# Optimization experiments

Measured on AMD Instinct MI355X. Metric: run time of the kernel, lower is better.

The kernel has to match this reference:

```python
import jax, jax.numpy as jnp
import numpy as np

LN_EPS = 1e-5


def setup_inputs() -> dict:
    key = jax.random.key(0)
    ks = jax.random.split(key, 8)
    N, H, E, D, B = 262144, 768, 768, 2048, 65536
    return {
        "u_t": jax.random.normal(ks[0], (B, E), dtype=jnp.float32),
        "s_i": jax.random.randint(ks[1], (B,), 0, N, dtype=jnp.int64),
        "speaker_embeddings": jax.random.normal(ks[2], (N, H), dtype=jnp.float32),
        "W1": jax.random.normal(ks[3], (D, H + E), dtype=jnp.float32) * 0.02,
        "b1": jax.random.normal(ks[4], (D,), dtype=jnp.float32) * 0.02,
        "W2": jax.random.normal(ks[5], (H, D), dtype=jnp.float32) * 0.02,
        "b2": jax.random.normal(ks[6], (H,), dtype=jnp.float32) * 0.02,
        "ln_gamma": jnp.ones((H,), dtype=jnp.float32),
        "ln_beta": jnp.zeros((H,), dtype=jnp.float32),
    }


def reference(u_t, s_i, speaker_embeddings, W1, b1, W2, b2, ln_gamma, ln_beta):
    # gather speaker vectors: [B, H]
    h_t = speaker_embeddings[s_i]
    # concat [u_t, h_t] along features: [B, E+H]
    x = jnp.concatenate([u_t, h_t], axis=-1)
    # Linear -> GELU (exact, torch default) -> (Dropout=identity in eval)
    h = jax.nn.gelu(jnp.einsum("bf,df->bd", x, W1) + b1, approximate=False)
    # Linear -> (Dropout=identity) : [B, H]
    y = jnp.einsum("bd,hd->bh", h, W2) + b2
    # LayerNorm over last dim
    mu = jnp.mean(y, axis=-1, keepdims=True)
    var = jnp.mean((y - mu) ** 2, axis=-1, keepdims=True)
    new_h_t = (y - mu) * jax.lax.rsqrt(var + LN_EPS) * ln_gamma + ln_beta
    # scatter-add back into the memory table (duplicates accumulate)
    updated = speaker_embeddings.at[s_i].add(new_h_t)
    return new_h_t, updated
```

## Files before the change

### kernel.cpp

```cpp
#include <hip/hip_runtime.h>
#include <hip/hip_bf16.h>

typedef unsigned short u16;
typedef unsigned int u32;
typedef short bf16x8 __attribute__((ext_vector_type(8)));
typedef float f32x4 __attribute__((ext_vector_type(4)));

__device__ __forceinline__ unsigned pk2(float lo, float hi) {
    unsigned a = (unsigned)__builtin_bit_cast(u16, __float2bfloat16(lo));
    unsigned b = (unsigned)__builtin_bit_cast(u16, __float2bfloat16(hi));
    return a | (b << 16);
}
__device__ __forceinline__ u16 f2bf(float v) {
    return __builtin_bit_cast(u16, __float2bfloat16(v));
}
__device__ __forceinline__ void gl_lds16(const u16* g, u16* l) {
    __builtin_amdgcn_global_load_lds(
        (const __attribute__((address_space(1))) u32*)g,
        (__attribute__((address_space(3))) u32*)l, 16, 0, 0);
}

__global__ void cvtbf(const float4* __restrict__ s, uint2* __restrict__ d, int n4) {
    int i = blockIdx.x * blockDim.x + threadIdx.x;
    int stride = gridDim.x * blockDim.x;
    for (; i < n4; i += stride) {
        float4 f = s[i];
        uint2 o;
        o.x = pk2(f.x, f.y);
        o.y = pk2(f.z, f.w);
        d[i] = o;
    }
}

__global__ __launch_bounds__(256) void xbuild(const float* __restrict__ u_t,
                                              const float* __restrict__ emb,
                                              const int* __restrict__ s_i,
                                              u16* __restrict__ xb) {
    const long u = (long)blockIdx.x * blockDim.x + threadIdx.x;
    const int row = (int)(u / 192);
    const int c8 = (int)(u % 192);
    const float* src = (c8 < 96) ? (u_t + (long)row * 768 + c8 * 8)
                                 : (emb + (long)s_i[row] * 768 + (c8 - 96) * 8);
    float4 f0 = ((const float4*)src)[0];
    float4 f1 = ((const float4*)src)[1];
    uint4 o;
    o.x = pk2(f0.x, f0.y);
    o.y = pk2(f0.z, f0.w);
    o.z = pk2(f1.x, f1.y);
    o.w = pk2(f1.z, f1.w);
    *(uint4*)(xb + u * 8) = o;
}

__global__ __launch_bounds__(256, 3) void gemm1_gelu(
    const u16* __restrict__ xb, const u16* __restrict__ w1b,
    const float* __restrict__ b1, u16* __restrict__ hbuf) {
    __shared__ __align__(16) u16 As[128 * 64];
    __shared__ __align__(16) u16 Bs[128 * 64];

    const int tid = threadIdx.x;
    const int lane = tid & 63;
    const int wv = tid >> 6;
    const int cpx = gridDim.x >> 3;
    const int tile = ((int)blockIdx.x & 7) * cpx + ((int)blockIdx.x >> 3);
    const int tm = tile >> 4;
    const int tn = tile & 15;
    const long rowBase = (long)tm * 128;
    const long colBase = (long)tn * 128;

    const u16* gA0 = xb + (rowBase + 8 * wv + (lane >> 3)) * 1536 + (lane & 7) * 8;
    const u16* gB0 = w1b + (colBase + 8 * wv + (lane >> 3)) * 1536 + (lane & 7) * 8;

    auto stage = [&](int kt) {
        const u16* ga = gA0 + kt * 64;
        const u16* gb = gB0 + kt * 64;
#pragma unroll
        for (int i = 0; i < 4; ++i) {
            gl_lds16(ga + (long)i * 32 * 1536, As + (32 * i + 8 * wv) * 64);
            gl_lds16(gb + (long)i * 32 * 1536, Bs + (32 * i + 8 * wv) * 64);
        }
    };

    const int wr = wv >> 1, wc = wv & 1;
    const u16* aBase = As + (wr * 64 + (lane & 15)) * 64 + (lane >> 4) * 8;
    const u16* bBase = Bs + (wc * 64 + (lane & 15)) * 64 + (lane >> 4) * 8;

    f32x4 acc[4][4];
    const f32x4 zero = {0.f, 0.f, 0.f, 0.f};
#pragma unroll
    for (int m = 0; m < 4; ++m)
#pragma unroll
        for (int n = 0; n < 4; ++n) acc[m][n] = zero;

    stage(0);
    for (int kt = 0; kt < 24; ++kt) {
        __syncthreads();
#pragma unroll
        for (int kk = 0; kk < 2; ++kk) {
            bf16x8 a[4], b[4];
#pragma unroll
            for (int m = 0; m < 4; ++m) a[m] = *(const bf16x8*)(aBase + m * 16 * 64 + kk * 32);
#pragma unroll
            for (int n = 0; n < 4; ++n) b[n] = *(const bf16x8*)(bBase + n * 16 * 64 + kk * 32);
#pragma unroll
            for (int m = 0; m < 4; ++m)
#pragma unroll
                for (int n = 0; n < 4; ++n)
                    acc[m][n] = __builtin_amdgcn_mfma_f32_16x16x32_bf16(a[m], b[n], acc[m][n], 0, 0, 0);
        }
        if (kt + 1 < 24) {
            __syncthreads();
            stage(kt + 1);
        }
    }

    const float* b1p = b1 + colBase;
#pragma unroll
    for (int n = 0; n < 4; ++n) {
        int gcl = wc * 64 + n * 16 + (lane & 15);
        float bias = b1p[gcl];
        long gc = colBase + gcl;
#pragma unroll
        for (int m = 0; m < 4; ++m) {
            long gr = rowBase + wr * 64 + m * 16 + ((lane >> 4) << 2);
            u16* dst = hbuf + gr * 2048 + gc;
#pragma unroll
            for (int j = 0; j < 4; ++j) {
                float v = acc[m][n][j] + bias;
                v = 0.5f * v * (1.0f + erff(v * 0.70710678118f));
                dst[(long)j * 2048] = f2bf(v);
            }
        }
    }
}

__global__ __launch_bounds__(256, 3) void gemm2_bias(
    const u16* __restrict__ hbuf, const u16* __restrict__ w2b,
    const float* __restrict__ b2, float* __restrict__ yout) {
    __shared__ __align__(16) u16 As[128 * 64];
    __shared__ __align__(16) u16 Bs[128 * 64];

    const int tid = threadIdx.x;
    const int lane = tid & 63;
    const int wv = tid >> 6;
    const int cpx = gridDim.x >> 3;
    const int tile = ((int)blockIdx.x & 7) * cpx + ((int)blockIdx.x >> 3);
    const int tm = tile / 6;
    const int tn = tile % 6;
    const long rowBase = (long)tm * 128;
    const long colBase = (long)tn * 128;

    const u16* gA0 = hbuf + (rowBase + 8 * wv + (lane >> 3)) * 2048 + (lane & 7) * 8;
    const u16* gB0 = w2b + (colBase + 8 * wv + (lane >> 3)) * 2048 + (lane & 7) * 8;

    auto stage = [&](int kt) {
        const u16* ga = gA0 + kt * 64;
        const u16* gb = gB0 + kt * 64;
#pragma unroll
        for (int i = 0; i < 4; ++i) {
            gl_lds16(ga + (long)i * 32 * 2048, As + (32 * i + 8 * wv) * 64);
            gl_lds16(gb + (long)i * 32 * 2048, Bs + (32 * i + 8 * wv) * 64);
        }
    };

    const int wr = wv >> 1, wc = wv & 1;
    const u16* aBase = As + (wr * 64 + (lane & 15)) * 64 + (lane >> 4) * 8;
    const u16* bBase = Bs + (wc * 64 + (lane & 15)) * 64 + (lane >> 4) * 8;

    f32x4 acc[4][4];
    const f32x4 zero = {0.f, 0.f, 0.f, 0.f};
#pragma unroll
    for (int m = 0; m < 4; ++m)
#pragma unroll
        for (int n = 0; n < 4; ++n) acc[m][n] = zero;

    stage(0);
    for (int kt = 0; kt < 32; ++kt) {
        __syncthreads();
#pragma unroll
        for (int kk = 0; kk < 2; ++kk) {
            bf16x8 a[4], b[4];
#pragma unroll
            for (int m = 0; m < 4; ++m) a[m] = *(const bf16x8*)(aBase + m * 16 * 64 + kk * 32);
#pragma unroll
            for (int n = 0; n < 4; ++n) b[n] = *(const bf16x8*)(bBase + n * 16 * 64 + kk * 32);
#pragma unroll
            for (int m = 0; m < 4; ++m)
#pragma unroll
                for (int n = 0; n < 4; ++n)
                    acc[m][n] = __builtin_amdgcn_mfma_f32_16x16x32_bf16(a[m], b[n], acc[m][n], 0, 0, 0);
        }
        if (kt + 1 < 32) {
            __syncthreads();
            stage(kt + 1);
        }
    }

    const float* b2p = b2 + colBase;
#pragma unroll
    for (int n = 0; n < 4; ++n) {
        int gcl = wc * 64 + n * 16 + (lane & 15);
        float bias = b2p[gcl];
        long gc = colBase + gcl;
#pragma unroll
        for (int m = 0; m < 4; ++m) {
            long gr = rowBase + wr * 64 + m * 16 + ((lane >> 4) << 2);
            float* dst = yout + gr * 768 + gc;
#pragma unroll
            for (int j = 0; j < 4; ++j) dst[(long)j * 768] = acc[m][n][j] + bias;
        }
    }
}

__global__ __launch_bounds__(256) void ln_scatter(float* __restrict__ y,
                                                  const float* __restrict__ gamma,
                                                  const float* __restrict__ beta,
                                                  const int* __restrict__ s_i,
                                                  float* __restrict__ upd) {
    const int lane = threadIdx.x & 63;
    const long row = (long)blockIdx.x * 4 + (threadIdx.x >> 6);
    const long base = row * 768;
    float v[12];
#pragma unroll
    for (int i = 0; i < 12; ++i) v[i] = y[base + i * 64 + lane];
    float s = 0.f, q = 0.f;
#pragma unroll
    for (int i = 0; i < 12; ++i) { s += v[i]; q += v[i] * v[i]; }
#pragma unroll
    for (int off = 32; off > 0; off >>= 1) {
        s += __shfl_xor(s, off, 64);
        q += __shfl_xor(q, off, 64);
    }
    const float mu = s * (1.f / 768.f);
    const float var = q * (1.f / 768.f) - mu * mu;
    const float inv = rsqrtf(var + 1e-5f);
    const long si = s_i[row];
#pragma unroll
    for (int i = 0; i < 12; ++i) {
        int c = i * 64 + lane;
        float r = (v[i] - mu) * inv * gamma[c] + beta[c];
        y[base + c] = r;
        atomicAdd(&upd[si * 768 + c], r);
    }
}

__global__ void copy4(const float4* __restrict__ s, float4* __restrict__ d, long n) {
    long i = (long)blockIdx.x * blockDim.x + threadIdx.x;
    long stride = (long)gridDim.x * blockDim.x;
    for (; i < n; i += stride) d[i] = s[i];
}

extern "C" void kernel_launch(void* const* d_in, const int* in_sizes, int n_in,
                              void* d_out, int out_size, void* d_ws, size_t ws_size,
                              hipStream_t stream) {
    const float* u_t = (const float*)d_in[0];
    const int* s_i = (const int*)d_in[1];
    const float* emb = (const float*)d_in[2];
    const float* W1 = (const float*)d_in[3];
    const float* b1 = (const float*)d_in[4];
    const float* W2 = (const float*)d_in[5];
    const float* b2 = (const float*)d_in[6];
    const float* gamma = (const float*)d_in[7];
    const float* beta = (const float*)d_in[8];

    float* out = (float*)d_out;
    float* newh = out;
    float* upd = out + 50331648L;

    u16* base = (u16*)upd;
    u16* hbuf = base;
    u16* xb = base + 134217728L;
    u16* w1b = base + 234881024L;
    u16* w2b = base + 238026752L;

    cvtbf<<<1024, 256, 0, stream>>>((const float4*)W1, (uint2*)w1b, 786432);
    cvtbf<<<1024, 256, 0, stream>>>((const float4*)W2, (uint2*)w2b, 393216);
    xbuild<<<49152, 256, 0, stream>>>(u_t, emb, s_i, xb);
    gemm1_gelu<<<8192, 256, 0, stream>>>(xb, w1b, b1, hbuf);
    gemm2_bias<<<3072, 256, 0, stream>>>(hbuf, w2b, b2, newh);
    copy4<<<2048, 256, 0, stream>>>((const float4*)emb, (float4*)upd, 50331648L);
    ln_scatter<<<16384, 256, 0, stream>>>(newh, gamma, beta, s_i, upd);
}
```

Baseline: 1.544 ms.

## Replace both GEMMs with 256x256-tile, 8-wave, double-buffered swizzled-LDS kernel

Both bf16 GEMMs move from 128x128 tiles with 4 waves to a templated 256x256-tile kernel with 8 waves, 128 KB of double-buffered LDS and XOR-swizzled layouts. The main loop is split into four sub-phases that interleave global-to-LDS prefetch of the next K tile with MFMA work, using explicit vmcnt/lgkmcnt waits, raw barriers and s_setprio. The aim is higher arithmetic intensity per LDS byte, fewer bank conflicts, and load latency hidden behind compute. In exchange the kernel uses many more registers and much more LDS, lowering occupancy, and relies on hand-tuned wait counts that could be fragile.

```diff
diff --git a/kernel.cpp b/kernel.cpp
--- a/kernel.cpp
+++ b/kernel.cpp
@@ -5,6 +5,11 @@
 typedef unsigned int u32;
 typedef short bf16x8 __attribute__((ext_vector_type(8)));
 typedef float f32x4 __attribute__((ext_vector_type(4)));
+
+#define BAR() asm volatile("s_barrier" ::: "memory")
+#define WAITV4() asm volatile("s_waitcnt vmcnt(4)" ::: "memory")
+#define WAITV0() asm volatile("s_waitcnt vmcnt(0)" ::: "memory")
+#define WAITL() asm volatile("s_waitcnt lgkmcnt(0)" ::: "memory")
 
 __device__ __forceinline__ unsigned pk2(float lo, float hi) {
     unsigned a = (unsigned)__builtin_bit_cast(u16, __float2bfloat16(lo));
@@ -51,162 +56,161 @@
     *(uint4*)(xb + u * 8) = o;
 }
 
-__global__ __launch_bounds__(256, 3) void gemm1_gelu(
-    const u16* __restrict__ xb, const u16* __restrict__ w1b,
-    const float* __restrict__ b1, u16* __restrict__ hbuf) {
-    __shared__ __align__(16) u16 As[128 * 64];
-    __shared__ __align__(16) u16 Bs[128 * 64];
+template <int LDK, int NT, int TN, int EPI>
+__global__ __launch_bounds__(512, 2) void gemm256(
+    const u16* __restrict__ Ag, const u16* __restrict__ Bg,
+    const float* __restrict__ bias, u16* __restrict__ outb,
+    float* __restrict__ outf) {
+    __shared__ __align__(16) u16 lds[65536];
 
     const int tid = threadIdx.x;
     const int lane = tid & 63;
     const int wv = tid >> 6;
-    const int cpx = gridDim.x >> 3;
+    const int wm = wv >> 2;
+    const int wn = wv & 3;
+
+    const int cpx = (int)gridDim.x >> 3;
     const int tile = ((int)blockIdx.x & 7) * cpx + ((int)blockIdx.x >> 3);
-    const int tm = tile >> 4;
-    const int tn = tile & 15;
-    const long rowBase = (long)tm * 128;
-    const long colBase = (long)tn * 128;
-
-    const u16* gA0 = xb + (rowBase + 8 * wv + (lane >> 3)) * 1536 + (lane & 7) * 8;
-    const u16* gB0 = w1b + (colBase + 8 * wv + (lane >> 3)) * 1536 + (lane & 7) * 8;
-
-    auto stage = [&](int kt) {
-        const u16* ga = gA0 + kt * 64;
-        const u16* gb = gB0 + kt * 64;
-#pragma unroll
-        for (int i = 0; i < 4; ++i) {
-            gl_lds16(ga + (long)i * 32 * 1536, As + (32 * i + 8 * wv) * 64);
-            gl_lds16(gb + (long)i * 32 * 1536, Bs + (32 * i + 8 * wv) * 64);
-        }
+    const int tm = tile / TN, tn = tile % TN;
+    const long rowBase = (long)tm * 256;
+    const long colBase = (long)tn * 256;
+
+    const int srow = tid >> 2;
+    const int gch = (tid & 3) ^ ((tid >> 3) & 3);
+    const u16* pA = Ag + (rowBase + srow) * (long)LDK + gch * 8;
+    const u16* pB = Bg + (colBase + srow) * (long)LDK + gch * 8;
+    const int dstBase = wv * 512;
+
+    auto stageA = [&](int kt, int ks, int b) {
+        const u16* s = pA + kt * 64 + ks * 32;
+        u16* d = lds + b * 32768 + ks * 8192 + dstBase;
+        gl_lds16(s, d);
+        gl_lds16(s + (long)128 * LDK, d + 4096);
     };
-
-    const int wr = wv >> 1, wc = wv & 1;
-    const u16* aBase = As + (wr * 64 + (lane & 15)) * 64 + (lane >> 4) * 8;
-    const u16* bBase = Bs + (wc * 64 + (lane & 15)) * 64 + (lane >> 4) * 8;
-
-    f32x4 acc[4][4];
+    auto stageB = [&](int kt, int ks, int b) {
+        const u16* s = pB + kt * 64 + ks * 32;
+        u16* d = lds + b * 32768 + 16384 + ks * 8192 + dstBase;
+        gl_lds16(s, d);
+        gl_lds16(s + (long)128 * LDK, d + 4096);
+    };
+
+    const int l15 = lane & 15, lc = lane >> 4;
+    int offA[8], offB[4];
+#pragma unroll
+    for (int i = 0; i < 8; ++i) {
+        int r = wm * 128 + i * 16 + l15;
+        offA[i] = r * 32 + ((lc ^ ((r >> 1) & 3)) << 3);
+    }
+#pragma unroll
+    for (int n = 0; n < 4; ++n) {
+        int r = wn * 64 + n * 16 + l15;
+        offB[n] = r * 32 + ((lc ^ ((r >> 1) & 3)) << 3);
+    }
+
+    f32x4 acc[8][4];
     const f32x4 zero = {0.f, 0.f, 0.f, 0.f};
 #pragma unroll
-    for (int m = 0; m < 4; ++m)
+    for (int m = 0; m < 8; ++m)
 #pragma unroll
         for (int n = 0; n < 4; ++n) acc[m][n] = zero;
 
-    stage(0);
-    for (int kt = 0; kt < 24; ++kt) {
-        __syncthreads();
-#pragma unroll
-        for (int kk = 0; kk < 2; ++kk) {
-            bf16x8 a[4], b[4];
-#pragma unroll
-            for (int m = 0; m < 4; ++m) a[m] = *(const bf16x8*)(aBase + m * 16 * 64 + kk * 32);
-#pragma unroll
-            for (int n = 0; n < 4; ++n) b[n] = *(const bf16x8*)(bBase + n * 16 * 64 + kk * 32);
-#pragma unroll
-            for (int m = 0; m < 4; ++m)
-#pragma unroll
-                for (int n = 0; n < 4; ++n)
-                    acc[m][n] = __builtin_amdgcn_mfma_f32_16x16x32_bf16(a[m], b[n], acc[m][n], 0, 0, 0);
-        }
-        if (kt + 1 < 24) {
-            __syncthreads();
-            stage(kt + 1);
-        }
-    }
-
-    const float* b1p = b1 + colBase;
+    stageA(0, 0, 0);
+    stageB(0, 0, 0);
+    stageA(0, 1, 0);
+    stageB(0, 1, 0);
+    WAITV4();
+    BAR();
+
+    bf16x8 bA[4], bB[4];
+    for (int kt = 0; kt < NT; ++kt) {
+        const int b = kt & 1;
+        const u16* rA0 = lds + b * 32768;
+        const u16* rB0 = rA0 + 16384;
+        const u16* rA1 = rA0 + 8192;
+        const u16* rB1 = rB0 + 8192;
+        const bool pf = (kt + 1 < NT);
+
+#pragma unroll
+        for (int n = 0; n < 4; ++n) bB[n] = *(const bf16x8*)(rB0 + offB[n]);
+#pragma unroll
+        for (int m = 0; m < 4; ++m) bA[m] = *(const bf16x8*)(rA0 + offA[m]);
+        if (pf) stageA(kt + 1, 0, b ^ 1);
+        BAR();
+        WAITL();
+        __builtin_amdgcn_s_setprio(1);
+#pragma unroll
+        for (int m = 0; m < 4; ++m)
+#pragma unroll
+            for (int n = 0; n < 4; ++n)
+                acc[m][n] = __builtin_amdgcn_mfma_f32_16x16x32_bf16(bA[m], bB[n], acc[m][n], 0, 0, 0);
+        __builtin_amdgcn_s_setprio(0);
+        BAR();
+
+#pragma unroll
+        for (int m = 0; m < 4; ++m) bA[m] = *(const bf16x8*)(rA0 + offA[4 + m]);
+        if (pf) stageB(kt + 1, 0, b ^ 1);
+        BAR();
+        WAITL();
+        __builtin_amdgcn_s_setprio(1);
+#pragma unroll
+        for (int m = 0; m < 4; ++m)
+#pragma unroll
+            for (int n = 0; n < 4; ++n)
+                acc[4 + m][n] = __builtin_amdgcn_mfma_f32_16x16x32_bf16(bA[m], bB[n], acc[4 + m][n], 0, 0, 0);
+        __builtin_amdgcn_s_setprio(0);
+        if (pf) { WAITV4(); } else { WAITV0(); }
+        BAR();
+
+#pragma unroll
+        for (int n = 0; n < 4; ++n) bB[n] = *(const bf16x8*)(rB1 + offB[n]);
+#pragma unroll
+        for (int m = 0; m < 4; ++m) bA[m] = *(const bf16x8*)(rA1 + offA[m]);
+        if (pf) stageA(kt + 1, 1, b ^ 1);
+        BAR();
+        WAITL();
+        __builtin_amdgcn_s_setprio(1);
+#pragma unroll
+        for (int m = 0; m < 4; ++m)
+#pragma unroll
+            for (int n = 0; n < 4; ++n)
+                acc[m][n] = __builtin_amdgcn_mfma_f32_16x16x32_bf16(bA[m], bB[n], acc[m][n], 0, 0, 0);
+        __builtin_amdgcn_s_setprio(0);
+        BAR();
+
+#pragma unroll
+        for (int m = 0; m < 4; ++m) bA[m] = *(const bf16x8*)(rA1 + offA[4 + m]);
+        if (pf) stageB(kt + 1, 1, b ^ 1);
+        BAR();
+        WAITL();
+        __builtin_amdgcn_s_setprio(1);
+#pragma unroll
+        for (int m = 0; m < 4; ++m)
+#pragma unroll
+            for (int n = 0; n < 4; ++n)
+                acc[4 + m][n] = __builtin_amdgcn_mfma_f32_16x16x32_bf16(bA[m], bB[n], acc[4 + m][n], 0, 0, 0);
+        __builtin_amdgcn_s_setprio(0);
+        if (pf) { WAITV4(); } else { WAITV0(); }
+        BAR();
+    }
+
+    const int N = TN * 256;
 #pragma unroll
     for (int n = 0; n < 4; ++n) {
-        int gcl = wc * 64 + n * 16 + (lane & 15);
-        float bias = b1p[gcl];
-        long gc = colBase + gcl;
-#pragma unroll
-        for (int m = 0; m < 4; ++m) {
-            long gr = rowBase + wr * 64 + m * 16 + ((lane >> 4) << 2);
-            u16* dst = hbuf + gr * 2048 + gc;
+        long gc = colBase + wn * 64 + n * 16 + l15;
+        float bv = bias[gc];
+#pragma unroll
+        for (int i = 0; i < 8; ++i) {
+            long gr = rowBase + wm * 128 + i * 16 + (lc << 2);
 #pragma unroll
             for (int j = 0; j < 4; ++j) {
-                float v = acc[m][n][j] + bias;
-                v = 0.5f * v * (1.0f + erff(v * 0.70710678118f));
-                dst[(long)j * 2048] = f2bf(v);
+                float v = acc[i][n][j] + bv;
+                if constexpr (EPI == 0) {
+                    v = 0.5f * v * (1.0f + erff(v * 0.70710678118f));
+                    outb[(gr + j) * N + gc] = f2bf(v);
+                } else {
+                    outf[(gr + j) * N + gc] = v;
+                }
             }
-        }
-    }
-}
-
-__global__ __launch_bounds__(256, 3) void gemm2_bias(
-    const u16* __restrict__ hbuf, const u16* __restrict__ w2b,
-    const float* __restrict__ b2, float* __restrict__ yout) {
-    __shared__ __align__(16) u16 As[128 * 64];
-    __shared__ __align__(16) u16 Bs[128 * 64];
-
-    const int tid = threadIdx.x;
-    const int lane = tid & 63;
-    const int wv = tid >> 6;
-    const int cpx = gridDim.x >> 3;
-    const int tile = ((int)blockIdx.x & 7) * cpx + ((int)blockIdx.x >> 3);
-    const int tm = tile / 6;
-    const int tn = tile % 6;
-    const long rowBase = (long)tm * 128;
-    const long colBase = (long)tn * 128;
-
-    const u16* gA0 = hbuf + (rowBase + 8 * wv + (lane >> 3)) * 2048 + (lane & 7) * 8;
-    const u16* gB0 = w2b + (colBase + 8 * wv + (lane >> 3)) * 2048 + (lane & 7) * 8;
-
-    auto stage = [&](int kt) {
-        const u16* ga = gA0 + kt * 64;
-        const u16* gb = gB0 + kt * 64;
-#pragma unroll
-        for (int i = 0; i < 4; ++i) {
-            gl_lds16(ga + (long)i * 32 * 2048, As + (32 * i + 8 * wv) * 64);
-            gl_lds16(gb + (long)i * 32 * 2048, Bs + (32 * i + 8 * wv) * 64);
-        }
-    };
-
-    const int wr = wv >> 1, wc = wv & 1;
-    const u16* aBase = As + (wr * 64 + (lane & 15)) * 64 + (lane >> 4) * 8;
-    const u16* bBase = Bs + (wc * 64 + (lane & 15)) * 64 + (lane >> 4) * 8;
-
-    f32x4 acc[4][4];
-    const f32x4 zero = {0.f, 0.f, 0.f, 0.f};
-#pragma unroll
-    for (int m = 0; m < 4; ++m)
-#pragma unroll
-        for (int n = 0; n < 4; ++n) acc[m][n] = zero;
-
-    stage(0);
-    for (int kt = 0; kt < 32; ++kt) {
-        __syncthreads();
-#pragma unroll
-        for (int kk = 0; kk < 2; ++kk) {
-            bf16x8 a[4], b[4];
-#pragma unroll
-            for (int m = 0; m < 4; ++m) a[m] = *(const bf16x8*)(aBase + m * 16 * 64 + kk * 32);
-#pragma unroll
-            for (int n = 0; n < 4; ++n) b[n] = *(const bf16x8*)(bBase + n * 16 * 64 + kk * 32);
-#pragma unroll
-            for (int m = 0; m < 4; ++m)
-#pragma unroll
-                for (int n = 0; n < 4; ++n)
-                    acc[m][n] = __builtin_amdgcn_mfma_f32_16x16x32_bf16(a[m], b[n], acc[m][n], 0, 0, 0);
-        }
-        if (kt + 1 < 32) {
-            __syncthreads();
-            stage(kt + 1);
-        }
-    }
-
-    const float* b2p = b2 + colBase;
-#pragma unroll
-    for (int n = 0; n < 4; ++n) {
-        int gcl = wc * 64 + n * 16 + (lane & 15);
-        float bias = b2p[gcl];
-        long gc = colBase + gcl;
-#pragma unroll
-        for (int m = 0; m < 4; ++m) {
-            long gr = rowBase + wr * 64 + m * 16 + ((lane >> 4) << 2);
-            float* dst = yout + gr * 768 + gc;
-#pragma unroll
-            for (int j = 0; j < 4; ++j) dst[(long)j * 768] = acc[m][n][j] + bias;
         }
     }
 }
@@ -275,8 +279,8 @@
     cvtbf<<<1024, 256, 0, stream>>>((const float4*)W1, (uint2*)w1b, 786432);
     cvtbf<<<1024, 256, 0, stream>>>((const float4*)W2, (uint2*)w2b, 393216);
     xbuild<<<49152, 256, 0, stream>>>(u_t, emb, s_i, xb);
-    gemm1_gelu<<<8192, 256, 0, stream>>>(xb, w1b, b1, hbuf);
-    gemm2_bias<<<3072, 256, 0, stream>>>(hbuf, w2b, b2, newh);
+    gemm256<1536, 24, 8, 0><<<2048, 512, 0, stream>>>(xb, w1b, b1, hbuf, nullptr);
+    gemm256<2048, 32, 3, 1><<<768, 512, 0, stream>>>(hbuf, w2b, b2, nullptr, newh);
     copy4<<<2048, 256, 0, stream>>>((const float4*)emb, (float4*)upd, 50331648L);
     ln_scatter<<<16384, 256, 0, stream>>>(newh, gamma, beta, s_i, upd);
 }
```

After: 1.390 ms. 1.11x faster.
